# Kernel optimization log

Measured on AMD Instinct MI355X. Metric: run time of the kernel, lower is better.

## Reference

```python
import jax, jax.numpy as jnp
import numpy as np

N_NODES = 100000
N_EDGES = 1600000
D_IN = 256
D_OUT = 256


def setup_inputs() -> dict:
    key = jax.random.key(0)
    k1, k2, k3, k4, k5 = jax.random.split(key, 5)
    x = jax.random.normal(k1, (N_NODES, D_IN), dtype=jnp.float32)
    edge_src = jax.random.randint(k2, (N_EDGES,), 0, N_NODES, dtype=jnp.int32)
    edge_dst = jax.random.randint(k3, (N_EDGES,), 0, N_NODES, dtype=jnp.int32)
    edge_val = jax.random.uniform(k4, (N_EDGES,), dtype=jnp.float32)
    stdv = 1.0 / np.sqrt(D_OUT)
    weight = jax.random.uniform(k5, (D_IN, D_OUT), dtype=jnp.float32,
                                minval=-stdv, maxval=stdv)
    return {"x": x, "edge_src": edge_src, "edge_dst": edge_dst,
            "edge_val": edge_val, "weight": weight}


def reference(x, edge_src, edge_dst, edge_val, weight):
    # torch.spmm(adj, x): out[dst] += adj_val * x[src]
    msgs = x[edge_src] * edge_val[:, None]                     # [E, D_IN]
    agg = jax.ops.segment_sum(msgs, edge_dst,
                              num_segments=x.shape[0])         # [N, D_IN]
    # torch.mm(aggregated, weight)
    return agg @ weight                                        # [N, D_OUT]
```

## Files before the change

kernel.cpp:

```cpp
#include <hip/hip_runtime.h>
#include <hip/hip_bf16.h>

#define D 256
#define BDST 128
#define CAP 2560
#define TILE 6144
#define YROW 264

typedef __attribute__((ext_vector_type(8))) short short8;
typedef __attribute__((ext_vector_type(4))) float f32x4;

static __device__ __forceinline__ unsigned short f2bf(float f) {
    union { float f; unsigned u; } u; u.f = f;
    unsigned r = u.u + 0x7FFF + ((u.u >> 16) & 1);
    return (unsigned short)(r >> 16);
}

static __device__ __forceinline__ float bf2f(unsigned short b) {
    union { unsigned u; float f; } u; u.u = ((unsigned)b) << 16;
    return u.f;
}

static __device__ __forceinline__ unsigned cvtpk(float a, float b) {
    unsigned r;
    asm("v_cvt_pk_bf16_f32 %0, %1, %2" : "=v"(r) : "v"(a), "v"(b));
    return r;
}

__global__ __launch_bounds__(256) void prep_kernel(
    const float* __restrict__ W, unsigned short* __restrict__ wF,
    const int* __restrict__ edst, int* __restrict__ gcount,
    int n_edges, int nb) {
    int tid = threadIdx.x;
    if (blockIdx.x < 32) {
        int fid = blockIdx.x * 4 + (tid >> 6);
        int lane = tid & 63;
        int kt = fid >> 4, nt = fid & 15;
        int col = nt * 16 + (lane & 15);
        int k0 = kt * 32 + (lane >> 4) * 8;
        unsigned short frag[8];
#pragma unroll
        for (int j = 0; j < 8; ++j) frag[j] = f2bf(W[(k0 + j) * D + col]);
        *(short8*)(wF + ((size_t)fid * 64 + lane) * 8) = *(short8*)frag;
    } else {
        __shared__ int h[1024];
        for (int j = tid; j < nb; j += 256) h[j] = 0;
        __syncthreads();
        int i = (blockIdx.x - 32) * 256 + tid;
        int stride = (gridDim.x - 32) * 256;
        for (; i < n_edges; i += stride) atomicAdd(&h[edst[i] >> 7], 1);
        __syncthreads();
        for (int j = tid; j < nb; j += 256) {
            int v = h[j];
            if (v) atomicAdd(&gcount[j], v);
        }
    }
}

__global__ __launch_bounds__(1024) void scan_bucket_kernel(
    const int* __restrict__ gcount, int* __restrict__ offs,
    int* __restrict__ cursor, int nb) {
    __shared__ int t[1024];
    int tid = threadIdx.x;
    int c = (tid < nb) ? gcount[tid] : 0;
    t[tid] = c;
    __syncthreads();
    for (int off = 1; off < 1024; off <<= 1) {
        int v = (tid >= off) ? t[tid - off] : 0;
        __syncthreads();
        t[tid] += v;
        __syncthreads();
    }
    if (tid < nb) { int e = t[tid] - c; offs[tid] = e; cursor[tid] = e; }
}

__global__ __launch_bounds__(1024) void fill_ms_kernel(
    const int* __restrict__ esrc, const int* __restrict__ edst,
    const float* __restrict__ eval, int* __restrict__ cursor,
    int2* __restrict__ binned, int n_edges, int nb) {
    __shared__ int lhist[1024];
    __shared__ int lscan[1024];
    __shared__ int lbase[1024];
    __shared__ int lcur[1024];

    int tid = threadIdx.x;
    int tb = blockIdx.x * TILE;
    int m = n_edges - tb; if (m > TILE) m = TILE;

    int src[6], dst[6]; float val[6];
#pragma unroll
    for (int j = 0; j < 6; ++j) {
        int i = tid + j * 1024;
        if (i < m) { src[j] = esrc[tb + i]; dst[j] = edst[tb + i]; val[j] = eval[tb + i]; }
    }

    for (int j = tid; j < nb; j += 1024) lhist[j] = 0;
    __syncthreads();
#pragma unroll
    for (int j = 0; j < 6; ++j)
        if (tid + j * 1024 < m) atomicAdd(&lhist[dst[j] >> 7], 1);
    __syncthreads();

    int c = (tid < nb) ? lhist[tid] : 0;
    lscan[tid] = c;
    __syncthreads();
    for (int off = 1; off < 1024; off <<= 1) {
        int v = (tid >= off) ? lscan[tid - off] : 0;
        __syncthreads();
        lscan[tid] += v;
        __syncthreads();
    }
    if (tid < nb) {
        int lofs = lscan[tid] - c;
        int gbase = c ? atomicAdd(&cursor[tid], c) : 0;
        lbase[tid] = gbase - lofs;
        lcur[tid] = lofs;
    }
    __syncthreads();

#pragma unroll
    for (int j = 0; j < 6; ++j) {
        if (tid + j * 1024 < m) {
            int d = dst[j];
            int b = d >> 7;
            int pos = atomicAdd(&lcur[b], 1);
            binned[lbase[b] + pos] =
                make_int2(src[j] | ((d & (BDST - 1)) << 20), __float_as_int(val[j]));
        }
    }
}

__global__ __launch_bounds__(256) void gemm_kernel(
    const float* __restrict__ x, const unsigned short* __restrict__ wF,
    unsigned short* __restrict__ y, int n_nodes) {
    __shared__ unsigned short ytile[64 * YROW];

    const int tid  = threadIdx.x;
    const int lane = tid & 63;
    const int wave = tid >> 6;
    const int rsel = lane & 15;
    const int koff = (lane >> 4) * 8;
    const int brow = blockIdx.x * 64;

    int row = brow + wave * 16 + rsel;
    int rowc = row < n_nodes ? row : n_nodes - 1;
    const float* xp = x + (size_t)rowc * D + koff;

    short8 a[8];
#pragma unroll
    for (int kt = 0; kt < 8; ++kt) {
        f32x4 lo = *(const f32x4*)(xp + kt * 32);
        f32x4 hi = *(const f32x4*)(xp + kt * 32 + 4);
        union { unsigned u[4]; short8 s; } pk;
        pk.u[0] = cvtpk(lo[0], lo[1]);
        pk.u[1] = cvtpk(lo[2], lo[3]);
        pk.u[2] = cvtpk(hi[0], hi[1]);
        pk.u[3] = cvtpk(hi[2], hi[3]);
        a[kt] = pk.s;
    }

    f32x4 acc[16];
#pragma unroll
    for (int nt = 0; nt < 16; ++nt) acc[nt] = (f32x4){0.f, 0.f, 0.f, 0.f};

    const short8* wf = (const short8*)wF;
#pragma unroll
    for (int kt = 0; kt < 8; ++kt) {
#pragma unroll
        for (int nt = 0; nt < 16; ++nt) {
            short8 b = wf[(kt * 16 + nt) * 64 + lane];
            acc[nt] = __builtin_amdgcn_mfma_f32_16x16x32_bf16(a[kt], b, acc[nt], 0, 0, 0);
        }
    }

    int lrow0 = wave * 16 + (lane >> 4) * 4;
#pragma unroll
    for (int nt = 0; nt < 16; ++nt) {
        int ccol = nt * 16 + rsel;
#pragma unroll
        for (int i = 0; i < 4; ++i)
            ytile[(lrow0 + i) * YROW + ccol] = f2bf(acc[nt][i]);
    }
    __syncthreads();

#pragma unroll
    for (int it = 0; it < 8; ++it) {
        int r = it * 8 + (tid >> 5);
        int col = (tid & 31) * 8;
        int gr = brow + r;
        if (gr < n_nodes)
            *(short8*)(y + (size_t)gr * D + col) = *(const short8*)(&ytile[r * YROW + col]);
    }
}

__global__ __launch_bounds__(256) void bucket_gather_kernel(
    const unsigned short* __restrict__ y, const int* __restrict__ offs,
    const int* __restrict__ bend, const int2* __restrict__ binned,
    float* __restrict__ out, int n_nodes) {
    __shared__ int2 lcsr[CAP];
    __shared__ int lhist[BDST];
    __shared__ int lscan[BDST];
    __shared__ int lofs[BDST];
    __shared__ int lcur[BDST];

    int b = blockIdx.x;
    int tid = threadIdx.x;
    int beg = offs[b];
    int end = bend[b];
    int cnt = end - beg;
    int nch = cnt > 0 ? (cnt + CAP - 1) / CAP : 1;

    const int hw = tid >> 5;
    const int lane = tid & 31;
    const unsigned short* yl = y + lane * 8;

    for (int c = 0; c < nch; ++c) {
        int cb = beg + c * CAP;
        int ce = cb + CAP < end ? cb + CAP : end;
        int m = ce > cb ? ce - cb : 0;

        int2 ec[10];
#pragma unroll
        for (int j = 0; j < 10; ++j) {
            int i = tid + j * 256;
            if (i < m) ec[j] = binned[cb + i];
        }

        if (tid < BDST) lhist[tid] = 0;
        __syncthreads();
#pragma unroll
        for (int j = 0; j < 10; ++j)
            if (tid + j * 256 < m) atomicAdd(&lhist[(ec[j].x >> 20) & (BDST - 1)], 1);
        __syncthreads();
        if (tid < BDST) lscan[tid] = lhist[tid];
        __syncthreads();
        for (int off = 1; off < BDST; off <<= 1) {
            int v = 0;
            if (tid < BDST && tid >= off) v = lscan[tid - off];
            __syncthreads();
            if (tid < BDST) lscan[tid] += v;
            __syncthreads();
        }
        if (tid < BDST) {
            int e = lscan[tid] - lhist[tid];
            lofs[tid] = e;
            lcur[tid] = e;
        }
        __syncthreads();
#pragma unroll
        for (int j = 0; j < 10; ++j) {
            if (tid + j * 256 < m) {
                int pos = atomicAdd(&lcur[(ec[j].x >> 20) & (BDST - 1)], 1);
                lcsr[pos] = ec[j];
            }
        }
        __syncthreads();

        for (int dl = hw; dl < BDST; dl += 8) {
            int d = b * BDST + dl;
            if (d >= n_nodes) break;
            int i0 = lofs[dl];
            int i1 = lcur[dl];
            float acc[8] = {0.f, 0.f, 0.f, 0.f, 0.f, 0.f, 0.f, 0.f};
            int i = i0;
            for (; i + 4 <= i1; i += 4) {
                int2 e0 = lcsr[i];
                int2 e1 = lcsr[i + 1];
                int2 e2 = lcsr[i + 2];
                int2 e3 = lcsr[i + 3];
                short8 r0 = *(const short8*)(yl + (size_t)(e0.x & 0xFFFFF) * D);
                short8 r1 = *(const short8*)(yl + (size_t)(e1.x & 0xFFFFF) * D);
                short8 r2 = *(const short8*)(yl + (size_t)(e2.x & 0xFFFFF) * D);
                short8 r3 = *(const short8*)(yl + (size_t)(e3.x & 0xFFFFF) * D);
                float v0 = __int_as_float(e0.y), v1 = __int_as_float(e1.y);
                float v2 = __int_as_float(e2.y), v3 = __int_as_float(e3.y);
#pragma unroll
                for (int j = 0; j < 8; ++j) {
                    acc[j] += v0 * bf2f((unsigned short)r0[j]);
                    acc[j] += v1 * bf2f((unsigned short)r1[j]);
                    acc[j] += v2 * bf2f((unsigned short)r2[j]);
                    acc[j] += v3 * bf2f((unsigned short)r3[j]);
                }
            }
            for (; i < i1; ++i) {
                int2 e0 = lcsr[i];
                float v0 = __int_as_float(e0.y);
                short8 r0 = *(const short8*)(yl + (size_t)(e0.x & 0xFFFFF) * D);
#pragma unroll
                for (int j = 0; j < 8; ++j) acc[j] += v0 * bf2f((unsigned short)r0[j]);
            }
            float* op = out + (size_t)d * D + lane * 8;
            if (c == 0) {
                *(f32x4*)(op)     = (f32x4){acc[0], acc[1], acc[2], acc[3]};
                *(f32x4*)(op + 4) = (f32x4){acc[4], acc[5], acc[6], acc[7]};
            } else {
                f32x4 o0 = *(f32x4*)(op);
                f32x4 o1 = *(f32x4*)(op + 4);
                o0[0] += acc[0]; o0[1] += acc[1]; o0[2] += acc[2]; o0[3] += acc[3];
                o1[0] += acc[4]; o1[1] += acc[5]; o1[2] += acc[6]; o1[3] += acc[7];
                *(f32x4*)(op)     = o0;
                *(f32x4*)(op + 4) = o1;
            }
        }
        __syncthreads();
    }
}

extern "C" void kernel_launch(void* const* d_in, const int* in_sizes, int n_in,
                              void* d_out, int out_size, void* d_ws, size_t ws_size,
                              hipStream_t stream) {
    const float* x    = (const float*)d_in[0];
    const int*   esrc = (const int*)d_in[1];
    const int*   edst = (const int*)d_in[2];
    const float* eval = (const float*)d_in[3];
    const float* W    = (const float*)d_in[4];
    float* out = (float*)d_out;

    const int n_nodes = in_sizes[0] / D;
    const int n_edges = in_sizes[1];
    const int nb = (n_nodes + BDST - 1) / BDST;

    char* ws = (char*)d_ws;
    unsigned short* y  = (unsigned short*)ws;  ws += (size_t)n_nodes * D * 2;
    unsigned short* wF = (unsigned short*)ws;  ws += (size_t)D * D * 2;
    int*  gcount  = (int*)ws;                  ws += 4096;
    int*  offs    = (int*)ws;                  ws += 4096;
    int*  cursor  = (int*)ws;                  ws += 4096;
    int2* binned  = (int2*)ws;                 ws += (size_t)n_edges * 8;

    hipMemsetAsync(gcount, 0, (size_t)nb * sizeof(int), stream);

    prep_kernel<<<256, 256, 0, stream>>>(W, wF, edst, gcount, n_edges, nb);

    scan_bucket_kernel<<<1, 1024, 0, stream>>>(gcount, offs, cursor, nb);

    const int ntiles = (n_edges + TILE - 1) / TILE;
    fill_ms_kernel<<<ntiles, 1024, 0, stream>>>(esrc, edst, eval, cursor, binned, n_edges, nb);

    gemm_kernel<<<(n_nodes + 63) / 64, 256, 0, stream>>>(x, wF, y, n_nodes);

    bucket_gather_kernel<<<nb, 256, 0, stream>>>(y, offs, cursor, binned, out, n_nodes);
}
```

Before: 242.9 us.

## Fold bucket scan into fill and gather kernels; widen GEMM tile to 128 rows

Removes the single-block scan kernel launch. Each fill block now redundantly scans the global bucket counts, and each gather block computes its own start offset by reduction. The memset is widened to 8192 bytes so it also zeroes the cursor array, which now holds relative offsets. The GEMM processes 128 rows per block with two row groups per wave, sharing each B fragment load across two MFMAs, and writes output in two column phases through a smaller LDS tile. The trade-off is redundant scan work in every fill block, plus the gather prefix sum, which grows with the bucket index.

```diff
diff --git a/kernel.cpp b/kernel.cpp
--- a/kernel.cpp
+++ b/kernel.cpp
@@ -5,7 +5,7 @@
 #define BDST 128
 #define CAP 2560
 #define TILE 6144
-#define YROW 264
+#define YR 136
 
 typedef __attribute__((ext_vector_type(8))) short short8;
 typedef __attribute__((ext_vector_type(4))) float f32x4;
@@ -57,33 +57,29 @@
     }
 }
 
-__global__ __launch_bounds__(1024) void scan_bucket_kernel(
-    const int* __restrict__ gcount, int* __restrict__ offs,
-    int* __restrict__ cursor, int nb) {
-    __shared__ int t[1024];
-    int tid = threadIdx.x;
-    int c = (tid < nb) ? gcount[tid] : 0;
-    t[tid] = c;
-    __syncthreads();
-    for (int off = 1; off < 1024; off <<= 1) {
-        int v = (tid >= off) ? t[tid - off] : 0;
-        __syncthreads();
-        t[tid] += v;
-        __syncthreads();
-    }
-    if (tid < nb) { int e = t[tid] - c; offs[tid] = e; cursor[tid] = e; }
-}
-
 __global__ __launch_bounds__(1024) void fill_ms_kernel(
     const int* __restrict__ esrc, const int* __restrict__ edst,
-    const float* __restrict__ eval, int* __restrict__ cursor,
-    int2* __restrict__ binned, int n_edges, int nb) {
+    const float* __restrict__ eval, const int* __restrict__ gcount,
+    int* __restrict__ cursor, int2* __restrict__ binned,
+    int n_edges, int nb) {
     __shared__ int lhist[1024];
     __shared__ int lscan[1024];
     __shared__ int lbase[1024];
     __shared__ int lcur[1024];
 
     int tid = threadIdx.x;
+
+    int gc = (tid < nb) ? gcount[tid] : 0;
+    lscan[tid] = gc;
+    __syncthreads();
+    for (int off = 1; off < 1024; off <<= 1) {
+        int v = (tid >= off) ? lscan[tid - off] : 0;
+        __syncthreads();
+        lscan[tid] += v;
+        __syncthreads();
+    }
+    int goff = lscan[tid] - gc;
+
     int tb = blockIdx.x * TILE;
     int m = n_edges - tb; if (m > TILE) m = TILE;
 
@@ -112,8 +108,8 @@
     }
     if (tid < nb) {
         int lofs = lscan[tid] - c;
-        int gbase = c ? atomicAdd(&cursor[tid], c) : 0;
-        lbase[tid] = gbase - lofs;
+        int g = c ? atomicAdd(&cursor[tid], c) : 0;
+        lbase[tid] = goff + g - lofs;
         lcur[tid] = lofs;
     }
     __syncthreads();
@@ -130,83 +126,108 @@
     }
 }
 
-__global__ __launch_bounds__(256) void gemm_kernel(
+__global__ __launch_bounds__(256, 3) void gemm_kernel(
     const float* __restrict__ x, const unsigned short* __restrict__ wF,
     unsigned short* __restrict__ y, int n_nodes) {
-    __shared__ unsigned short ytile[64 * YROW];
+    __shared__ unsigned short ytile[128 * YR];
 
     const int tid  = threadIdx.x;
     const int lane = tid & 63;
     const int wave = tid >> 6;
     const int rsel = lane & 15;
     const int koff = (lane >> 4) * 8;
-    const int brow = blockIdx.x * 64;
-
-    int row = brow + wave * 16 + rsel;
-    int rowc = row < n_nodes ? row : n_nodes - 1;
-    const float* xp = x + (size_t)rowc * D + koff;
-
-    short8 a[8];
-#pragma unroll
-    for (int kt = 0; kt < 8; ++kt) {
-        f32x4 lo = *(const f32x4*)(xp + kt * 32);
-        f32x4 hi = *(const f32x4*)(xp + kt * 32 + 4);
-        union { unsigned u[4]; short8 s; } pk;
-        pk.u[0] = cvtpk(lo[0], lo[1]);
-        pk.u[1] = cvtpk(lo[2], lo[3]);
-        pk.u[2] = cvtpk(hi[0], hi[1]);
-        pk.u[3] = cvtpk(hi[2], hi[3]);
-        a[kt] = pk.s;
-    }
-
-    f32x4 acc[16];
-#pragma unroll
-    for (int nt = 0; nt < 16; ++nt) acc[nt] = (f32x4){0.f, 0.f, 0.f, 0.f};
+    const int brow = blockIdx.x * 128;
+    const int wrow = brow + wave * 32;
+
+    short8 a[2][8];
+#pragma unroll
+    for (int rg = 0; rg < 2; ++rg) {
+        int row = wrow + rg * 16 + rsel;
+        int rowc = row < n_nodes ? row : n_nodes - 1;
+        const float* xp = x + (size_t)rowc * D + koff;
+#pragma unroll
+        for (int kt = 0; kt < 8; ++kt) {
+            f32x4 lo = *(const f32x4*)(xp + kt * 32);
+            f32x4 hi = *(const f32x4*)(xp + kt * 32 + 4);
+            union { unsigned u[4]; short8 s; } pk;
+            pk.u[0] = cvtpk(lo[0], lo[1]);
+            pk.u[1] = cvtpk(lo[2], lo[3]);
+            pk.u[2] = cvtpk(hi[0], hi[1]);
+            pk.u[3] = cvtpk(hi[2], hi[3]);
+            a[rg][kt] = pk.s;
+        }
+    }
 
     const short8* wf = (const short8*)wF;
 #pragma unroll
-    for (int kt = 0; kt < 8; ++kt) {
-#pragma unroll
-        for (int nt = 0; nt < 16; ++nt) {
-            short8 b = wf[(kt * 16 + nt) * 64 + lane];
-            acc[nt] = __builtin_amdgcn_mfma_f32_16x16x32_bf16(a[kt], b, acc[nt], 0, 0, 0);
-        }
-    }
-
-    int lrow0 = wave * 16 + (lane >> 4) * 4;
-#pragma unroll
-    for (int nt = 0; nt < 16; ++nt) {
-        int ccol = nt * 16 + rsel;
-#pragma unroll
-        for (int i = 0; i < 4; ++i)
-            ytile[(lrow0 + i) * YROW + ccol] = f2bf(acc[nt][i]);
-    }
-    __syncthreads();
-
-#pragma unroll
-    for (int it = 0; it < 8; ++it) {
-        int r = it * 8 + (tid >> 5);
-        int col = (tid & 31) * 8;
-        int gr = brow + r;
-        if (gr < n_nodes)
-            *(short8*)(y + (size_t)gr * D + col) = *(const short8*)(&ytile[r * YROW + col]);
+    for (int ph = 0; ph < 2; ++ph) {
+        f32x4 acc[2][8];
+#pragma unroll
+        for (int rg = 0; rg < 2; ++rg)
+#pragma unroll
+            for (int n = 0; n < 8; ++n) acc[rg][n] = (f32x4){0.f, 0.f, 0.f, 0.f};
+
+#pragma unroll
+        for (int kt = 0; kt < 8; ++kt) {
+#pragma unroll
+            for (int n = 0; n < 8; ++n) {
+                short8 bfr = wf[(kt * 16 + ph * 8 + n) * 64 + lane];
+                acc[0][n] = __builtin_amdgcn_mfma_f32_16x16x32_bf16(a[0][kt], bfr, acc[0][n], 0, 0, 0);
+                acc[1][n] = __builtin_amdgcn_mfma_f32_16x16x32_bf16(a[1][kt], bfr, acc[1][n], 0, 0, 0);
+            }
+        }
+
+#pragma unroll
+        for (int rg = 0; rg < 2; ++rg) {
+            int lrow0 = wave * 32 + rg * 16 + (lane >> 4) * 4;
+#pragma unroll
+            for (int n = 0; n < 8; ++n) {
+                int lcol = n * 16 + rsel;
+#pragma unroll
+                for (int i = 0; i < 4; ++i)
+                    ytile[(lrow0 + i) * YR + lcol] = f2bf(acc[rg][n][i]);
+            }
+        }
+        __syncthreads();
+
+#pragma unroll
+        for (int it = 0; it < 8; ++it) {
+            int idx = it * 256 + tid;
+            int r = idx >> 4;
+            int ch = idx & 15;
+            int gr = brow + r;
+            if (gr < n_nodes)
+                *(short8*)(y + (size_t)gr * D + ph * 128 + ch * 8) =
+                    *(const short8*)(&ytile[r * YR + ch * 8]);
+        }
+        __syncthreads();
     }
 }
 
 __global__ __launch_bounds__(256) void bucket_gather_kernel(
-    const unsigned short* __restrict__ y, const int* __restrict__ offs,
-    const int* __restrict__ bend, const int2* __restrict__ binned,
-    float* __restrict__ out, int n_nodes) {
+    const unsigned short* __restrict__ y, const int* __restrict__ gcount,
+    const int2* __restrict__ binned, float* __restrict__ out,
+    int n_nodes, int nb) {
     __shared__ int2 lcsr[CAP];
     __shared__ int lhist[BDST];
     __shared__ int lscan[BDST];
     __shared__ int lofs[BDST];
     __shared__ int lcur[BDST];
+    __shared__ int t[256];
 
     int b = blockIdx.x;
     int tid = threadIdx.x;
-    int beg = offs[b];
-    int end = bend[b];
+
+    int partial = 0;
+    for (int j = tid; j < b; j += 256) partial += gcount[j];
+    t[tid] = partial;
+    __syncthreads();
+    for (int off = 128; off > 0; off >>= 1) {
+        if (tid < off) t[tid] += t[tid + off];
+        __syncthreads();
+    }
+    int beg = t[0];
+    int end = beg + gcount[b];
     int cnt = end - beg;
     int nch = cnt > 0 ? (cnt + CAP - 1) / CAP : 1;
 
@@ -324,20 +345,18 @@
     unsigned short* y  = (unsigned short*)ws;  ws += (size_t)n_nodes * D * 2;
     unsigned short* wF = (unsigned short*)ws;  ws += (size_t)D * D * 2;
     int*  gcount  = (int*)ws;                  ws += 4096;
-    int*  offs    = (int*)ws;                  ws += 4096;
     int*  cursor  = (int*)ws;                  ws += 4096;
     int2* binned  = (int2*)ws;                 ws += (size_t)n_edges * 8;
 
-    hipMemsetAsync(gcount, 0, (size_t)nb * sizeof(int), stream);
+    hipMemsetAsync(gcount, 0, 8192, stream);
 
     prep_kernel<<<256, 256, 0, stream>>>(W, wF, edst, gcount, n_edges, nb);
 
-    scan_bucket_kernel<<<1, 1024, 0, stream>>>(gcount, offs, cursor, nb);
-
     const int ntiles = (n_edges + TILE - 1) / TILE;
-    fill_ms_kernel<<<ntiles, 1024, 0, stream>>>(esrc, edst, eval, cursor, binned, n_edges, nb);
-
-    gemm_kernel<<<(n_nodes + 63) / 64, 256, 0, stream>>>(x, wF, y, n_nodes);
-
-    bucket_gather_kernel<<<nb, 256, 0, stream>>>(y, offs, cursor, binned, out, n_nodes);
-}
+    fill_ms_kernel<<<ntiles, 1024, 0, stream>>>(esrc, edst, eval, gcount, cursor,
+                                                binned, n_edges, nb);
+
+    gemm_kernel<<<(n_nodes + 127) / 128, 256, 0, stream>>>(x, wF, y, n_nodes);
+
+    bucket_gather_kernel<<<nb, 256, 0, stream>>>(y, gcount, binned, out, n_nodes, nb);
+}
```

Result: slower. 256.3 us (+5.5%).
